# Kernel tuning notes

Hardware: AMD Instinct MI355X
Metric: run time of the kernel (lower is better)

## Reference

```python
import jax, jax.numpy as jnp
import numpy as np

DIM = 64
N_ITER = 2
NUM_USR = 50000
NUM_ENT = 200000
NUM_REL = 32
N_NEIGHBOR = 16
BATCH = 4096


def setup_inputs() -> dict:
    key = jax.random.key(0)
    ks = jax.random.split(key, 12)
    u = jax.random.randint(ks[0], (BATCH,), 0, NUM_USR)
    v = jax.random.randint(ks[1], (BATCH,), 0, NUM_ENT)
    adj = jax.random.randint(ks[2], (NUM_ENT, N_NEIGHBOR), 0, NUM_ENT)
    rel_adj = jax.random.randint(ks[3], (NUM_ENT, N_NEIGHBOR), 0, NUM_REL + 1)
    usr_emb = jax.random.normal(ks[4], (NUM_USR, DIM), dtype=jnp.float32)
    ent_emb = jax.random.normal(ks[5], (NUM_ENT, DIM), dtype=jnp.float32)
    rel_emb = jax.random.normal(ks[6], (NUM_REL + 1, DIM), dtype=jnp.float32)
    # per-hop aggregator Linear(dim, dim) weights (applied as x @ W + b)
    scale = 1.0 / np.sqrt(DIM)
    W0 = jax.random.uniform(ks[7], (DIM, DIM), jnp.float32, -scale, scale)
    b0 = jax.random.uniform(ks[8], (DIM,), jnp.float32, -scale, scale)
    W1 = jax.random.uniform(ks[9], (DIM, DIM), jnp.float32, -scale, scale)
    b1 = jax.random.uniform(ks[10], (DIM,), jnp.float32, -scale, scale)
    return {"u": u, "v": v, "adj": adj, "rel_adj": rel_adj,
            "usr_emb": usr_emb, "ent_emb": ent_emb, "rel_emb": rel_emb,
            "W0": W0, "b0": b0, "W1": W1, "b1": b1}


def reference(u, v, adj, rel_adj, usr_emb, ent_emb, rel_emb, W0, b0, W1, b1):
    B = u.shape[0]
    user = usr_emb[u]  # [B, D]

    # multi-hop neighbor index expansion
    entities = [v[:, None]]            # hop h: [B, n^h]
    relations = []
    for h in range(N_ITER):
        ne = adj[entities[h]].reshape(B, -1)      # [B, n^(h+1)]
        nr = rel_adj[entities[h]].reshape(B, -1)
        entities.append(ne)
        relations.append(nr)

    ent_vecs = [ent_emb[e] for e in entities]     # [B, n^h, D]
    rel_vecs = [rel_emb[r] for r in relations]

    Ws, bs = [W0, W1], [b0, b1]
    for i in range(N_ITER):
        act = jnp.tanh if i == N_ITER - 1 else jax.nn.sigmoid
        nxt = []
        for hop in range(N_ITER - i):
            sv = ent_vecs[hop]                                        # [B, m, D]
            nv = ent_vecs[hop + 1].reshape(B, -1, N_NEIGHBOR, DIM)    # [B, m, n, D]
            nr = rel_vecs[hop].reshape(B, -1, N_NEIGHBOR, DIM)        # [B, m, n, D]
            # user-relation attention over neighbors
            scores = jnp.einsum('bd,bmnd->bmn', user, nr)
            attn = jax.nn.softmax(scores, axis=-1)
            agg = jnp.einsum('bmn,bmnd->bmd', attn, nv)
            out = act((sv + agg) @ Ws[i] + bs[i])
            nxt.append(out)
        ent_vecs = nxt

    item = ent_vecs[0].reshape(B, DIM)
    return jax.nn.sigmoid(jnp.sum(user * item, axis=1))
```

## Files before the change

kernel.cpp:

```cpp
#include <hip/hip_runtime.h>

#define DIMN 64
#define NNB 16
#define NREL 33

__global__ __launch_bounds__(64, 4)
void kgs_kernel(const int* __restrict__ u, const int* __restrict__ v,
                const int* __restrict__ adj, const int* __restrict__ rel_adj,
                const float* __restrict__ usr_emb, const float* __restrict__ ent_emb,
                const float* __restrict__ rel_emb,
                const float* __restrict__ W0, const float* __restrict__ b0,
                const float* __restrict__ W1, const float* __restrict__ b1,
                float* __restrict__ out)
{
    const int b = blockIdx.x;
    const int d = threadIdx.x;
    const int n16 = d & 15;

    __shared__ __align__(16) float user_sh[DIMN];
    __shared__ float ur[NREL + 3];
    __shared__ float sv_sh[NNB * DIMN];
    __shared__ float h1_sh[NNB * DIMN];

    const int uu = u[b];
    const int vv = v[b];

    const float user_d = usr_emb[uu * DIMN + d];
    user_sh[d] = user_d;
    __syncthreads();

    if (d < NREL) {
        const float* re = rel_emb + d * DIMN;
        float acc = 0.f;
        #pragma unroll
        for (int k = 0; k < DIMN; k += 4) {
            const float4 uk = *(const float4*)(user_sh + k);
            const float4 rk = *(const float4*)(re + k);
            acc = fmaf(uk.x, rk.x, acc);
            acc = fmaf(uk.y, rk.y, acc);
            acc = fmaf(uk.z, rk.z, acc);
            acc = fmaf(uk.w, rk.w, acc);
        }
        ur[d] = acc;
    }
    __syncthreads();

    float w[DIMN];
    #pragma unroll
    for (int k = 0; k < DIMN; ++k) w[k] = W0[k * DIMN + d];
    const float b0d = b0[d];

    const int e1n = adj[vv * NNB + n16];
    const int r1n = rel_adj[vv * NNB + n16];

    for (int m = 0; m < NNB; ++m) {
        const int em = __builtin_amdgcn_readlane(e1n, m);
        const float sv = ent_emb[em * DIMN + d];
        sv_sh[m * DIMN + d] = sv;

        const int e2n = adj[em * NNB + n16];
        const int r2n = rel_adj[em * NNB + n16];

        const float s = ur[r2n];
        float mx = s;
        mx = fmaxf(mx, __shfl_xor(mx, 1));
        mx = fmaxf(mx, __shfl_xor(mx, 2));
        mx = fmaxf(mx, __shfl_xor(mx, 4));
        mx = fmaxf(mx, __shfl_xor(mx, 8));
        const float e = __expf(s - mx);
        float sum = e;
        sum += __shfl_xor(sum, 1);
        sum += __shfl_xor(sum, 2);
        sum += __shfl_xor(sum, 4);
        sum += __shfl_xor(sum, 8);
        const float attn = e / sum;

        float agg = 0.f;
        #pragma unroll
        for (int n = 0; n < NNB; ++n) {
            const int en = __builtin_amdgcn_readlane(e2n, n);
            const int ai = __builtin_amdgcn_readlane(__float_as_int(attn), n);
            agg = fmaf(__int_as_float(ai), ent_emb[en * DIMN + d], agg);
        }

        const float x = sv + agg;
        float o = b0d;
        #pragma unroll
        for (int k = 0; k < DIMN; ++k) {
            const int xi = __builtin_amdgcn_readlane(__float_as_int(x), k);
            o = fmaf(__int_as_float(xi), w[k], o);
        }
        h1_sh[m * DIMN + d] = 1.f / (1.f + __expf(-o));
    }
    __syncthreads();

    const float sv0 = ent_emb[vv * DIMN + d];
    const float s0 = ur[r1n];
    float mx0 = s0;
    mx0 = fmaxf(mx0, __shfl_xor(mx0, 1));
    mx0 = fmaxf(mx0, __shfl_xor(mx0, 2));
    mx0 = fmaxf(mx0, __shfl_xor(mx0, 4));
    mx0 = fmaxf(mx0, __shfl_xor(mx0, 8));
    const float e0 = __expf(s0 - mx0);
    float sum0 = e0;
    sum0 += __shfl_xor(sum0, 1);
    sum0 += __shfl_xor(sum0, 2);
    sum0 += __shfl_xor(sum0, 4);
    sum0 += __shfl_xor(sum0, 8);
    const float attn0 = e0 / sum0;

    float agg0 = 0.f;
    #pragma unroll
    for (int n = 0; n < NNB; ++n) {
        const int ai = __builtin_amdgcn_readlane(__float_as_int(attn0), n);
        agg0 = fmaf(__int_as_float(ai), sv_sh[n * DIMN + d], agg0);
    }
    const float x0 = sv0 + agg0;
    float o0 = b0d;
    #pragma unroll
    for (int k = 0; k < DIMN; ++k) {
        const int xi = __builtin_amdgcn_readlane(__float_as_int(x0), k);
        o0 = fmaf(__int_as_float(xi), w[k], o0);
    }
    const float h0 = 1.f / (1.f + __expf(-o0));

    #pragma unroll
    for (int k = 0; k < DIMN; ++k) w[k] = W1[k * DIMN + d];
    const float b1d = b1[d];

    float agg1 = 0.f;
    #pragma unroll
    for (int n = 0; n < NNB; ++n) {
        const int ai = __builtin_amdgcn_readlane(__float_as_int(attn0), n);
        agg1 = fmaf(__int_as_float(ai), h1_sh[n * DIMN + d], agg1);
    }
    const float x1 = h0 + agg1;
    float o1 = b1d;
    #pragma unroll
    for (int k = 0; k < DIMN; ++k) {
        const int xi = __builtin_amdgcn_readlane(__float_as_int(x1), k);
        o1 = fmaf(__int_as_float(xi), w[k], o1);
    }
    const float item_d = 1.f - 2.f / (1.f + __expf(2.f * o1));

    float p = user_d * item_d;
    p += __shfl_xor(p, 1);
    p += __shfl_xor(p, 2);
    p += __shfl_xor(p, 4);
    p += __shfl_xor(p, 8);
    p += __shfl_xor(p, 16);
    p += __shfl_xor(p, 32);
    if (d == 0) out[b] = 1.f / (1.f + __expf(-p));
}

extern "C" void kernel_launch(void* const* d_in, const int* in_sizes, int n_in,
                              void* d_out, int out_size, void* d_ws, size_t ws_size,
                              hipStream_t stream) {
    const int*   u       = (const int*)d_in[0];
    const int*   v       = (const int*)d_in[1];
    const int*   adj     = (const int*)d_in[2];
    const int*   rel_adj = (const int*)d_in[3];
    const float* usr_emb = (const float*)d_in[4];
    const float* ent_emb = (const float*)d_in[5];
    const float* rel_emb = (const float*)d_in[6];
    const float* W0      = (const float*)d_in[7];
    const float* b0      = (const float*)d_in[8];
    const float* W1      = (const float*)d_in[9];
    const float* b1      = (const float*)d_in[10];
    float* out = (float*)d_out;

    const int B = in_sizes[0];
    kgs_kernel<<<dim3(B), dim3(64), 0, stream>>>(u, v, adj, rel_adj, usr_emb, ent_emb,
                                                 rel_emb, W0, b0, W1, b1, out);
}
```

Before: 165.2 us.

## Batch hop-1 neighbour matmuls in registers and pack four samples per block

```diff
diff --git a/kernel.cpp b/kernel.cpp
--- a/kernel.cpp
+++ b/kernel.cpp
@@ -3,30 +3,36 @@
 #define DIMN 64
 #define NNB 16
 #define NREL 33
+#define WPB 4
 
-__global__ __launch_bounds__(64, 4)
+__device__ __forceinline__ float bcastf(float x, int lane) {
+    return __int_as_float(__builtin_amdgcn_readlane(__float_as_int(x), lane));
+}
+
+__global__ __launch_bounds__(64 * WPB, 4)
 void kgs_kernel(const int* __restrict__ u, const int* __restrict__ v,
                 const int* __restrict__ adj, const int* __restrict__ rel_adj,
                 const float* __restrict__ usr_emb, const float* __restrict__ ent_emb,
                 const float* __restrict__ rel_emb,
                 const float* __restrict__ W0, const float* __restrict__ b0,
                 const float* __restrict__ W1, const float* __restrict__ b1,
-                float* __restrict__ out)
+                float* __restrict__ out, int B)
 {
-    const int b = blockIdx.x;
-    const int d = threadIdx.x;
+    const int tid = threadIdx.x;
+    const int wid = tid >> 6;
+    const int d   = tid & 63;
+    int b = blockIdx.x * WPB + wid;
+    if (b >= B) b = B - 1;
     const int n16 = d & 15;
 
-    __shared__ __align__(16) float user_sh[DIMN];
-    __shared__ float ur[NREL + 3];
-    __shared__ float sv_sh[NNB * DIMN];
-    __shared__ float h1_sh[NNB * DIMN];
+    __shared__ __align__(16) float user_sh[WPB][DIMN];
+    __shared__ float ur_sh[WPB][NREL + 7];
 
     const int uu = u[b];
     const int vv = v[b];
 
     const float user_d = usr_emb[uu * DIMN + d];
-    user_sh[d] = user_d;
+    user_sh[wid][d] = user_d;
     __syncthreads();
 
     if (d < NREL) {
@@ -34,123 +40,118 @@
         float acc = 0.f;
         #pragma unroll
         for (int k = 0; k < DIMN; k += 4) {
-            const float4 uk = *(const float4*)(user_sh + k);
+            const float4 uk = *(const float4*)(&user_sh[wid][k]);
             const float4 rk = *(const float4*)(re + k);
             acc = fmaf(uk.x, rk.x, acc);
             acc = fmaf(uk.y, rk.y, acc);
             acc = fmaf(uk.z, rk.z, acc);
             acc = fmaf(uk.w, rk.w, acc);
         }
-        ur[d] = acc;
+        ur_sh[wid][d] = acc;
     }
     __syncthreads();
 
-    float w[DIMN];
-    #pragma unroll
-    for (int k = 0; k < DIMN; ++k) w[k] = W0[k * DIMN + d];
+    const int e1n = adj[vv * NNB + n16];
+    const int r1n = rel_adj[vv * NNB + n16];
     const float b0d = b0[d];
 
-    const int e1n = adj[vv * NNB + n16];
-    const int r1n = rel_adj[vv * NNB + n16];
+    float sv_r[NNB];
+    float xs[NNB];
 
+    #pragma unroll
     for (int m = 0; m < NNB; ++m) {
         const int em = __builtin_amdgcn_readlane(e1n, m);
         const float sv = ent_emb[em * DIMN + d];
-        sv_sh[m * DIMN + d] = sv;
 
         const int e2n = adj[em * NNB + n16];
         const int r2n = rel_adj[em * NNB + n16];
 
-        const float s = ur[r2n];
-        float mx = s;
-        mx = fmaxf(mx, __shfl_xor(mx, 1));
-        mx = fmaxf(mx, __shfl_xor(mx, 2));
-        mx = fmaxf(mx, __shfl_xor(mx, 4));
-        mx = fmaxf(mx, __shfl_xor(mx, 8));
-        const float e = __expf(s - mx);
+        const float e = __expf(ur_sh[wid][r2n]);
         float sum = e;
         sum += __shfl_xor(sum, 1);
         sum += __shfl_xor(sum, 2);
         sum += __shfl_xor(sum, 4);
         sum += __shfl_xor(sum, 8);
-        const float attn = e / sum;
+        const float attn = e * __builtin_amdgcn_rcpf(sum);
 
         float agg = 0.f;
         #pragma unroll
         for (int n = 0; n < NNB; ++n) {
             const int en = __builtin_amdgcn_readlane(e2n, n);
-            const int ai = __builtin_amdgcn_readlane(__float_as_int(attn), n);
-            agg = fmaf(__int_as_float(ai), ent_emb[en * DIMN + d], agg);
+            agg = fmaf(bcastf(attn, n), ent_emb[en * DIMN + d], agg);
         }
+        sv_r[m] = sv;
+        xs[m]   = sv + agg;
+    }
 
-        const float x = sv + agg;
-        float o = b0d;
+    float o[NNB];
+    #pragma unroll
+    for (int m = 0; m < NNB; ++m) o[m] = b0d;
+
+    #pragma unroll 4
+    for (int k = 0; k < DIMN; ++k) {
+        const float wk = W0[k * DIMN + d];
         #pragma unroll
-        for (int k = 0; k < DIMN; ++k) {
-            const int xi = __builtin_amdgcn_readlane(__float_as_int(x), k);
-            o = fmaf(__int_as_float(xi), w[k], o);
-        }
-        h1_sh[m * DIMN + d] = 1.f / (1.f + __expf(-o));
+        for (int m = 0; m < NNB; ++m)
+            o[m] = fmaf(bcastf(xs[m], k), wk, o[m]);
     }
-    __syncthreads();
+
+    float h1[NNB];
+    #pragma unroll
+    for (int m = 0; m < NNB; ++m)
+        h1[m] = 1.f / (1.f + __expf(-o[m]));
 
     const float sv0 = ent_emb[vv * DIMN + d];
-    const float s0 = ur[r1n];
-    float mx0 = s0;
-    mx0 = fmaxf(mx0, __shfl_xor(mx0, 1));
-    mx0 = fmaxf(mx0, __shfl_xor(mx0, 2));
-    mx0 = fmaxf(mx0, __shfl_xor(mx0, 4));
-    mx0 = fmaxf(mx0, __shfl_xor(mx0, 8));
-    const float e0 = __expf(s0 - mx0);
+    const float e0 = __expf(ur_sh[wid][r1n]);
     float sum0 = e0;
     sum0 += __shfl_xor(sum0, 1);
     sum0 += __shfl_xor(sum0, 2);
     sum0 += __shfl_xor(sum0, 4);
     sum0 += __shfl_xor(sum0, 8);
-    const float attn0 = e0 / sum0;
+    const float attn0 = e0 * __builtin_amdgcn_rcpf(sum0);
 
-    float agg0 = 0.f;
+    float agg0 = 0.f, agg1 = 0.f;
     #pragma unroll
     for (int n = 0; n < NNB; ++n) {
-        const int ai = __builtin_amdgcn_readlane(__float_as_int(attn0), n);
-        agg0 = fmaf(__int_as_float(ai), sv_sh[n * DIMN + d], agg0);
+        const float an = bcastf(attn0, n);
+        agg0 = fmaf(an, sv_r[n], agg0);
+        agg1 = fmaf(an, h1[n],  agg1);
     }
+
     const float x0 = sv0 + agg0;
-    float o0 = b0d;
-    #pragma unroll
-    for (int k = 0; k < DIMN; ++k) {
-        const int xi = __builtin_amdgcn_readlane(__float_as_int(x0), k);
-        o0 = fmaf(__int_as_float(xi), w[k], o0);
+    {
+        float a0 = 0.f, a1 = 0.f, a2 = 0.f, a3 = 0.f;
+        for (int k = 0; k < DIMN; k += 4) {
+            const float* wr = W0 + k * DIMN;
+            a0 = fmaf(bcastf(x0, k + 0), wr[d], a0);
+            a1 = fmaf(bcastf(x0, k + 1), wr[DIMN + d], a1);
+            a2 = fmaf(bcastf(x0, k + 2), wr[2 * DIMN + d], a2);
+            a3 = fmaf(bcastf(x0, k + 3), wr[3 * DIMN + d], a3);
+        }
+        const float o0 = b0d + ((a0 + a1) + (a2 + a3));
+        const float h0 = 1.f / (1.f + __expf(-o0));
+
+        const float x1 = h0 + agg1;
+        float c0 = 0.f, c1 = 0.f, c2 = 0.f, c3 = 0.f;
+        for (int k = 0; k < DIMN; k += 4) {
+            const float* wr = W1 + k * DIMN;
+            c0 = fmaf(bcastf(x1, k + 0), wr[d], c0);
+            c1 = fmaf(bcastf(x1, k + 1), wr[DIMN + d], c1);
+            c2 = fmaf(bcastf(x1, k + 2), wr[2 * DIMN + d], c2);
+            c3 = fmaf(bcastf(x1, k + 3), wr[3 * DIMN + d], c3);
+        }
+        const float o1 = b1[d] + ((c0 + c1) + (c2 + c3));
+        const float item_d = 1.f - 2.f / (1.f + __expf(2.f * o1));
+
+        float p = user_d * item_d;
+        p += __shfl_xor(p, 1);
+        p += __shfl_xor(p, 2);
+        p += __shfl_xor(p, 4);
+        p += __shfl_xor(p, 8);
+        p += __shfl_xor(p, 16);
+        p += __shfl_xor(p, 32);
+        if (d == 0) out[b] = 1.f / (1.f + __expf(-p));
     }
-    const float h0 = 1.f / (1.f + __expf(-o0));
-
-    #pragma unroll
-    for (int k = 0; k < DIMN; ++k) w[k] = W1[k * DIMN + d];
-    const float b1d = b1[d];
-
-    float agg1 = 0.f;
-    #pragma unroll
-    for (int n = 0; n < NNB; ++n) {
-        const int ai = __builtin_amdgcn_readlane(__float_as_int(attn0), n);
-        agg1 = fmaf(__int_as_float(ai), h1_sh[n * DIMN + d], agg1);
-    }
-    const float x1 = h0 + agg1;
-    float o1 = b1d;
-    #pragma unroll
-    for (int k = 0; k < DIMN; ++k) {
-        const int xi = __builtin_amdgcn_readlane(__float_as_int(x1), k);
-        o1 = fmaf(__int_as_float(xi), w[k], o1);
-    }
-    const float item_d = 1.f - 2.f / (1.f + __expf(2.f * o1));
-
-    float p = user_d * item_d;
-    p += __shfl_xor(p, 1);
-    p += __shfl_xor(p, 2);
-    p += __shfl_xor(p, 4);
-    p += __shfl_xor(p, 8);
-    p += __shfl_xor(p, 16);
-    p += __shfl_xor(p, 32);
-    if (d == 0) out[b] = 1.f / (1.f + __expf(-p));
 }
 
 extern "C" void kernel_launch(void* const* d_in, const int* in_sizes, int n_in,
@@ -170,6 +171,8 @@
     float* out = (float*)d_out;
 
     const int B = in_sizes[0];
-    kgs_kernel<<<dim3(B), dim3(64), 0, stream>>>(u, v, adj, rel_adj, usr_emb, ent_emb,
-                                                 rel_emb, W0, b0, W1, b1, out);
+    const int grid = (B + WPB - 1) / WPB;
+    kgs_kernel<<<dim3(grid), dim3(64 * WPB), 0, stream>>>(u, v, adj, rel_adj, usr_emb,
+                                                          ent_emb, rel_emb, W0, b0, W1, b1,
+                                                          out, B);
 }
```

Measured after the change: 175.4 us. 1.06x slower.
